# Kernel optimization log

Measured on AMD Instinct MI355X. Metric: run time of the kernel, lower is better.

Reference implementation:

```python
import jax, jax.numpy as jnp
import numpy as np
import math

BINSIZE = 200
WIDTH = 100000
BINWIDTH = WIDTH // BINSIZE  # 500
WINDOW0 = 0


def setup_inputs() -> dict:
    key = jax.random.key(0)
    ks = jax.random.split(key, 8)
    n_regions, n_clusters = 5000, 20
    n_regions_oi, n_fragments, n_cells = 200, 2_000_000, 100_000
    return {
        "baseline_weight": jax.random.normal(ks[0], (n_regions, BINWIDTH), dtype=jnp.float32),
        "delta_logit_weight": jax.random.normal(ks[1], (n_regions, n_clusters, BINWIDTH), dtype=jnp.float32),
        "inside": jnp.ones((1,), dtype=jnp.float32),
        "regions_oi": jax.random.randint(ks[2], (n_regions_oi,), 0, n_regions),
        "coordinates": jax.random.randint(ks[3], (n_fragments, 2), 0, WIDTH),
        "local_region_ix": jax.random.randint(ks[4], (n_fragments,), 0, n_regions_oi),
        "local_cell_ix": jax.random.randint(ks[5], (n_fragments,), 0, n_cells),
        "labels": jax.random.randint(ks[6], (n_cells,), 0, n_clusters),
    }


def reference(baseline_weight, delta_logit_weight, inside, regions_oi,
              coordinates, local_region_ix, local_cell_ix, labels):
    # Embedding lookups: [R_oi, 1, B] + [R_oi, C, B]
    unnormalized = baseline_weight[regions_oi][:, None, :] + delta_logit_weight[regions_oi]
    # log-softmax over bins, converted to density (divide by binsize)
    heights = jax.nn.log_softmax(unnormalized, axis=-1) - math.log(BINSIZE)
    # bin indices for left/right coordinates
    bin_left = (coordinates[:, 0] - WINDOW0) // BINSIZE
    bin_right = (coordinates[:, 1] - WINDOW0) // BINSIZE
    # triple-indexed gather: (region, cluster-of-cell, bin) -> scalar logprob
    logprob_left = heights[local_region_ix, labels[local_cell_ix], bin_left]
    # inside/outside term for the right coordinate
    match = (bin_left == bin_right).astype(heights.dtype)  # [N]
    s = jax.nn.sigmoid(inside)  # [1]
    logprob_inside = jnp.log(s) - math.log(BINWIDTH)
    logprob_outside = jnp.log(1.0 - s) - math.log(WIDTH - BINWIDTH)
    logprob_right = logprob_inside * match + logprob_outside * (1.0 - match)  # [N]
    return jnp.stack([logprob_left, logprob_right], axis=-1)  # [N, 2]
```

## Files before the change

kernel.cpp:

```cpp
#include <hip/hip_runtime.h>
#include <hip/hip_bf16.h>
#include <hip/hip_fp16.h>
#include <math.h>
#include <string.h>

#define BINSIZE 200
#define BINW 500
#define NCLUST 20
#define NREG_OI 200
#define LOG_BINSIZE   5.2983173665480363f
#define LOG_BINWIDTH  6.2146080984221914f
#define LOG_OUTWIDTH 11.5079131920500050f


typedef int   vint2   __attribute__((ext_vector_type(2)));
typedef int   vint4   __attribute__((ext_vector_type(4)));
typedef float vfloat4 __attribute__((ext_vector_type(4)));

#define HBLOCKS 1000
#define LBLOCKS 98

__global__ void heights_kernel(const float* __restrict__ baseline,
                               const float* __restrict__ delta,
                               const int*   __restrict__ regions_oi,
                               const int*   __restrict__ labels,
                               _Float16*    __restrict__ heights,
                               unsigned char* __restrict__ labels8,
                               int ncells)
{
    if (blockIdx.x >= HBLOCKS) {
        const int t = (blockIdx.x - HBLOCKS) * 256 + threadIdx.x;
        const int i0 = t * 4;
        if (i0 + 3 < ncells) {
            const vint4 l = __builtin_nontemporal_load((const vint4*)labels + t);
            unsigned packed = (unsigned)(l.x & 0xff)
                            | ((unsigned)(l.y & 0xff) << 8)
                            | ((unsigned)(l.z & 0xff) << 16)
                            | ((unsigned)(l.w & 0xff) << 24);
            *(unsigned*)(labels8 + i0) = packed;
        } else {
            for (int i = i0; i < ncells; ++i) labels8[i] = (unsigned char)labels[i];
        }
        return;
    }

    const int wave = blockIdx.x * 4 + (threadIdx.x >> 6);
    const int lane = threadIdx.x & 63;
    if (wave >= NREG_OI * NCLUST) return;

    const int r = wave / NCLUST;
    const int c = wave % NCLUST;
    const int g = regions_oi[r];

    const float* bptr = baseline + (size_t)g * BINW;
    const float* dptr = delta + ((size_t)g * NCLUST + c) * BINW;

    float u[8];
    float m = -INFINITY;
#pragma unroll
    for (int k = 0; k < 8; ++k) {
        const int b = lane + 64 * k;
        u[k] = (b < BINW)
             ? (bptr[b] + __builtin_nontemporal_load(dptr + b))
             : -INFINITY;
        m = fmaxf(m, u[k]);
    }
#pragma unroll
    for (int off = 32; off > 0; off >>= 1)
        m = fmaxf(m, __shfl_xor(m, off));

    float s = 0.f;
#pragma unroll
    for (int k = 0; k < 8; ++k) {
        const int b = lane + 64 * k;
        if (b < BINW) s += __expf(u[k] - m);
    }
#pragma unroll
    for (int off = 32; off > 0; off >>= 1)
        s += __shfl_xor(s, off);

    const float lse = m + __logf(s);
    _Float16* hptr = heights + (size_t)wave * BINW;
#pragma unroll
    for (int k = 0; k < 8; ++k) {
        const int b = lane + 64 * k;
        if (b < BINW) hptr[b] = (_Float16)(u[k] - lse - LOG_BINSIZE);
    }
}

__global__ __launch_bounds__(256)
void frag_kernel(const _Float16* __restrict__ heights,
                 const unsigned char* __restrict__ labels8,
                 const int*      __restrict__ coords,
                 const int*      __restrict__ lrix,
                 const int*      __restrict__ lcix,
                 const float*    __restrict__ inside,
                 float*          __restrict__ out,
                 int N)
{
    const int q  = blockIdx.x * blockDim.x + threadIdx.x;
    const int f0 = q * 4;
    if (f0 >= N) return;

    const float x  = inside[0];
    const float sg = 1.f / (1.f + __expf(-x));
    const float lp_in  = __logf(sg)       - LOG_BINWIDTH;
    const float lp_out = __logf(1.f - sg) - LOG_OUTWIDTH;

    if (f0 + 3 < N) {
        const vint4 c01 = __builtin_nontemporal_load((const vint4*)coords + 2 * q);
        const vint4 c23 = __builtin_nontemporal_load((const vint4*)coords + 2 * q + 1);
        const vint4 rr  = __builtin_nontemporal_load((const vint4*)lrix + q);
        const vint4 ce  = __builtin_nontemporal_load((const vint4*)lcix + q);

        const int lab0 = (int)labels8[ce.x];
        const int lab1 = (int)labels8[ce.y];
        const int lab2 = (int)labels8[ce.z];
        const int lab3 = (int)labels8[ce.w];

        const unsigned bl0 = (unsigned)c01.x / (unsigned)BINSIZE;
        const unsigned br0 = (unsigned)c01.y / (unsigned)BINSIZE;
        const unsigned bl1 = (unsigned)c01.z / (unsigned)BINSIZE;
        const unsigned br1 = (unsigned)c01.w / (unsigned)BINSIZE;
        const unsigned bl2 = (unsigned)c23.x / (unsigned)BINSIZE;
        const unsigned br2 = (unsigned)c23.y / (unsigned)BINSIZE;
        const unsigned bl3 = (unsigned)c23.z / (unsigned)BINSIZE;
        const unsigned br3 = (unsigned)c23.w / (unsigned)BINSIZE;

        const float h0 = (float)heights[(rr.x * NCLUST + lab0) * BINW + (int)bl0];
        const float h1 = (float)heights[(rr.y * NCLUST + lab1) * BINW + (int)bl1];
        const float h2 = (float)heights[(rr.z * NCLUST + lab2) * BINW + (int)bl2];
        const float h3 = (float)heights[(rr.w * NCLUST + lab3) * BINW + (int)bl3];

        vfloat4 o01, o23;
        o01.x = h0;
        o01.y = (bl0 == br0) ? lp_in : lp_out;
        o01.z = h1;
        o01.w = (bl1 == br1) ? lp_in : lp_out;
        o23.x = h2;
        o23.y = (bl2 == br2) ? lp_in : lp_out;
        o23.z = h3;
        o23.w = (bl3 == br3) ? lp_in : lp_out;
        __builtin_nontemporal_store(o01, (vfloat4*)out + 2 * q);
        __builtin_nontemporal_store(o23, (vfloat4*)out + 2 * q + 1);
    } else {
        for (int f = f0; f < N; ++f) {
            const unsigned bl = (unsigned)coords[2 * f]     / (unsigned)BINSIZE;
            const unsigned br = (unsigned)coords[2 * f + 1] / (unsigned)BINSIZE;
            const int lab = (int)labels8[lcix[f]];
            const float h = (float)heights[(lrix[f] * NCLUST + lab) * BINW + (int)bl];
            out[2 * f]     = h;
            out[2 * f + 1] = (bl == br) ? lp_in : lp_out;
        }
    }
}

extern "C" void kernel_launch(void* const* d_in, const int* in_sizes, int n_in,
                              void* d_out, int out_size, void* d_ws, size_t ws_size,
                              hipStream_t stream) {
    const float* baseline   = (const float*)d_in[0];
    const float* delta      = (const float*)d_in[1];
    const float* inside     = (const float*)d_in[2];
    const int*   regions_oi = (const int*)d_in[3];
    const int*   coords     = (const int*)d_in[4];
    const int*   lrix       = (const int*)d_in[5];
    const int*   lcix       = (const int*)d_in[6];
    const int*   labels     = (const int*)d_in[7];
    float*       out        = (float*)d_out;

    _Float16*      heights = (_Float16*)d_ws;
    unsigned char* labels8 = (unsigned char*)d_ws + (4u << 20);

    const int N      = in_sizes[4] / 2;
    const int ncells = in_sizes[7];
    const int Nquad  = (N + 3) / 4;

    heights_kernel<<<HBLOCKS + LBLOCKS, 256, 0, stream>>>(
        baseline, delta, regions_oi, labels, heights, labels8, ncells);

    frag_kernel<<<(Nquad + 255) / 256, 256, 0, stream>>>(
        heights, labels8, coords, lrix, lcix, inside, out, N);
}
```

Before: 283.0 us.

## Precompute per-fragment cluster labels in heights kernel instead of frag kernel

The label gather (labels[lcix[f]]) moves out of the fragment kernel and into extra blocks of the heights kernel, which run alongside the softmax work and write a packed byte array of per-fragment labels. The fragment kernel then reads one packed uint per four fragments instead of loading lcix and doing a dependent random byte gather. The aim is to hide the random gather latency by overlapping it with the compute-light heights pass and to shorten the dependent load chain in the fragment kernel. In exchange it adds a 2M-byte intermediate write and read, and the random gather now hits the 400KB int labels array rather than the 100KB byte copy.

Result: no change. 284.4 us (+0.5%).

```diff
diff --git a/kernel.cpp b/kernel.cpp
--- a/kernel.cpp
+++ b/kernel.cpp
@@ -18,28 +18,30 @@
 typedef float vfloat4 __attribute__((ext_vector_type(4)));
 
 #define HBLOCKS 1000
-#define LBLOCKS 98
 
 __global__ void heights_kernel(const float* __restrict__ baseline,
                                const float* __restrict__ delta,
                                const int*   __restrict__ regions_oi,
                                const int*   __restrict__ labels,
+                               const int*   __restrict__ lcix,
                                _Float16*    __restrict__ heights,
-                               unsigned char* __restrict__ labels8,
-                               int ncells)
+                               unsigned char* __restrict__ fraglab8,
+                               int N)
 {
     if (blockIdx.x >= HBLOCKS) {
-        const int t = (blockIdx.x - HBLOCKS) * 256 + threadIdx.x;
+        const int t  = (blockIdx.x - HBLOCKS) * 256 + threadIdx.x;
         const int i0 = t * 4;
-        if (i0 + 3 < ncells) {
-            const vint4 l = __builtin_nontemporal_load((const vint4*)labels + t);
-            unsigned packed = (unsigned)(l.x & 0xff)
-                            | ((unsigned)(l.y & 0xff) << 8)
-                            | ((unsigned)(l.z & 0xff) << 16)
-                            | ((unsigned)(l.w & 0xff) << 24);
-            *(unsigned*)(labels8 + i0) = packed;
+        if (i0 >= N) return;
+        if (i0 + 3 < N) {
+            const vint4 ce = __builtin_nontemporal_load((const vint4*)lcix + t);
+            const unsigned l0 = (unsigned)labels[ce.x] & 0xff;
+            const unsigned l1 = (unsigned)labels[ce.y] & 0xff;
+            const unsigned l2 = (unsigned)labels[ce.z] & 0xff;
+            const unsigned l3 = (unsigned)labels[ce.w] & 0xff;
+            *(unsigned*)(fraglab8 + i0) = l0 | (l1 << 8) | (l2 << 16) | (l3 << 24);
         } else {
-            for (int i = i0; i < ncells; ++i) labels8[i] = (unsigned char)labels[i];
+            for (int i = i0; i < N; ++i)
+                fraglab8[i] = (unsigned char)labels[lcix[i]];
         }
         return;
     }
@@ -90,10 +92,9 @@
 
 __global__ __launch_bounds__(256)
 void frag_kernel(const _Float16* __restrict__ heights,
-                 const unsigned char* __restrict__ labels8,
+                 const unsigned char* __restrict__ fraglab8,
                  const int*      __restrict__ coords,
                  const int*      __restrict__ lrix,
-                 const int*      __restrict__ lcix,
                  const float*    __restrict__ inside,
                  float*          __restrict__ out,
                  int N)
@@ -111,12 +112,12 @@
         const vint4 c01 = __builtin_nontemporal_load((const vint4*)coords + 2 * q);
         const vint4 c23 = __builtin_nontemporal_load((const vint4*)coords + 2 * q + 1);
         const vint4 rr  = __builtin_nontemporal_load((const vint4*)lrix + q);
-        const vint4 ce  = __builtin_nontemporal_load((const vint4*)lcix + q);
-
-        const int lab0 = (int)labels8[ce.x];
-        const int lab1 = (int)labels8[ce.y];
-        const int lab2 = (int)labels8[ce.z];
-        const int lab3 = (int)labels8[ce.w];
+        const unsigned labp =
+            __builtin_nontemporal_load((const unsigned*)fraglab8 + q);
+        const int lab0 = (int)(labp & 0xff);
+        const int lab1 = (int)((labp >> 8) & 0xff);
+        const int lab2 = (int)((labp >> 16) & 0xff);
+        const int lab3 = (int)(labp >> 24);
 
         const unsigned bl0 = (unsigned)c01.x / (unsigned)BINSIZE;
         const unsigned br0 = (unsigned)c01.y / (unsigned)BINSIZE;
@@ -147,7 +148,7 @@
         for (int f = f0; f < N; ++f) {
             const unsigned bl = (unsigned)coords[2 * f]     / (unsigned)BINSIZE;
             const unsigned br = (unsigned)coords[2 * f + 1] / (unsigned)BINSIZE;
-            const int lab = (int)labels8[lcix[f]];
+            const int lab = (int)fraglab8[f];
             const float h = (float)heights[(lrix[f] * NCLUST + lab) * BINW + (int)bl];
             out[2 * f]     = h;
             out[2 * f + 1] = (bl == br) ? lp_in : lp_out;
@@ -168,16 +169,16 @@
     const int*   labels     = (const int*)d_in[7];
     float*       out        = (float*)d_out;
 
-    _Float16*      heights = (_Float16*)d_ws;
-    unsigned char* labels8 = (unsigned char*)d_ws + (4u << 20);
+    _Float16*      heights  = (_Float16*)d_ws;
+    unsigned char* fraglab8 = (unsigned char*)d_ws + (4u << 20);
 
     const int N      = in_sizes[4] / 2;
-    const int ncells = in_sizes[7];
     const int Nquad  = (N + 3) / 4;
+    const int FBLOCKS = (Nquad + 255) / 256;
 
-    heights_kernel<<<HBLOCKS + LBLOCKS, 256, 0, stream>>>(
-        baseline, delta, regions_oi, labels, heights, labels8, ncells);
+    heights_kernel<<<HBLOCKS + FBLOCKS, 256, 0, stream>>>(
+        baseline, delta, regions_oi, labels, lcix, heights, fraglab8, N);
 
     frag_kernel<<<(Nquad + 255) / 256, 256, 0, stream>>>(
-        heights, labels8, coords, lrix, lcix, inside, out, N);
+        heights, fraglab8, coords, lrix, inside, out, N);
 }
```
